# Optimization experiments

Measured on AMD Instinct MI355X. Metric: run time of the kernel, lower is better.

The kernel has to match this reference:

```python
import jax, jax.numpy as jnp
import numpy as np

ATOL = 1e-06
RTOL = 1e-06

def setup_inputs() -> dict:
    key = jax.random.key(0)
    ks = jax.random.split(key, 8)
    u = lambda k, shape: jax.random.uniform(k, shape, jnp.float32, -0.05, 0.05)
    return {
        "x": jax.random.normal(ks[0], (4096, 32, 32, 3), jnp.float32),
        "W_lstm": u(ks[1], (3, 16)),      # input kernel, gates [i,f,c,o]
        "U_lstm": u(ks[2], (4, 16)),      # recurrent kernel
        "dw_kernel": u(ks[3], (27, 27, 3, 5)),  # depthwise (kh,kw,in_c,mult)
        "pw_kernel": u(ks[4], (15, 4)),   # pointwise
        "conv_bias": u(ks[5], (4,)),
        "W_td": u(ks[6], (4096, 10)),
        "W_sc": u(ks[7], (4096, 10)),
    }

def _lstm_td(x, W, U):
    # TimeDistributed LSTM: x (B,32,32,3) -> treat axis1 as TD batch, axis2 as time
    B = x.shape[0]
    seq = x.reshape(B * 32, 32, 3)          # (N, T, F)
    xs = jnp.transpose(seq, (1, 0, 2))      # (T, N, F)
    N = seq.shape[0]
    h0 = jnp.zeros((N, 4), x.dtype)
    c0 = jnp.zeros((N, 4), x.dtype)

    def step(carry, xt):
        h, c = carry
        z = xt @ W + h @ U                  # (N, 16)
        zi, zf, zc, zo = jnp.split(z, 4, axis=-1)
        i = jax.nn.elu(zi)                  # recurrent_activation='elu'
        f = jax.nn.elu(zf)
        c = f * c + i * jax.nn.softmax(zc, axis=-1)  # activation='softmax'
        o = jax.nn.elu(zo)
        h = o * jax.nn.softmax(c, axis=-1)
        return (h, c), h

    _, hs = jax.lax.scan(step, (h0, c0), xs)        # (T, N, 4)
    return jnp.transpose(hs, (1, 0, 2)).reshape(B, 32, 32, 4)

def _sep_conv(x, dw_kernel, pw_kernel, conv_bias):
    # depthwise: Keras (kh,kw,C,M) -> lax HWIO grouped (kh,kw,1,C*M), channel-major order
    dw = dw_kernel.reshape(27, 27, 1, 15)
    y = jax.lax.conv_general_dilated(
        x, dw, window_strides=(1, 1), padding='SAME',
        feature_group_count=3,
        dimension_numbers=('NHWC', 'HWIO', 'NHWC'))   # (B,32,32,15)
    y = jnp.einsum('bhwc,cf->bhwf', y, pw_kernel) + conv_bias
    return jax.nn.sigmoid(y)                          # (B,32,32,4)

def reference(x, W_lstm, U_lstm, dw_kernel, pw_kernel, conv_bias, W_td, W_sc):
    B = x.shape[0]
    td = _lstm_td(x, W_lstm, U_lstm).reshape(B, -1) @ W_td   # (B,10)
    sc = _sep_conv(x, dw_kernel, pw_kernel, conv_bias).reshape(B, -1) @ W_sc
    diff = jnp.abs(td - sc)
    tol = ATOL + RTOL * jnp.abs(sc)
    return diff <= tol
```

## Files before the change

kernel.cpp:

```cpp
#include <hip/hip_runtime.h>
#include <math.h>

#define TD_OFF 0
#define WTDR_OFF 40960
#define SC_OFF 81920
#define BG_BYTE_OFF 524288

typedef __bf16 bf16x8 __attribute__((ext_vector_type(8)));
typedef float f32x16 __attribute__((ext_vector_type(16)));
typedef float f32x2 __attribute__((ext_vector_type(2)));

union FragU { bf16x8 v; float4 f; };

__device__ __forceinline__ f32x16 mfma16(bf16x8 a, bf16x8 b, f32x16 c) {
    return __builtin_amdgcn_mfma_f32_32x32x16_bf16(a, b, c, 0, 0, 0);
}

__device__ __forceinline__ float eluf(float v) {
    return v > 0.f ? v : __expf(v) - 1.f;
}

__global__ __launch_bounds__(256) void prep(const float* __restrict__ dw,
                                            const float* __restrict__ pw,
                                            const float* __restrict__ Wtd,
                                            float* __restrict__ Wtdr,
                                            unsigned short* __restrict__ Bg) {
    int gid = blockIdx.x * 256 + threadIdx.x;
    if (gid < 40960) {
        int k = gid & 3;
        int r = gid >> 2;
        int row = r & 31; r >>= 5;
        int j = r % 10;
        int tt = r / 10;
        Wtdr[gid] = Wtd[(size_t)(row * 128 + tt * 4 + k) * 10 + j];
        return;
    }
    int g2 = gid - 40960;
    if (g2 >= 162 * 128) return;
    int n = g2 & 127;
    int s = g2 >> 7;
    int half = s & 1;
    int cd = s >> 1;
    int c = cd / 27, d = cd % 27;
    int w = n >> 2, f = n & 3;
    unsigned short* dsth = Bg + (size_t)s * 4096 + n * 16;
    unsigned short* dstl = dsth + 2048;
#pragma unroll
    for (int k = 0; k < 16; k++) {
        int xi = half * 16 + k;
        int dx = xi - w + 13;
        float v = 0.f;
        if (dx >= 0 && dx < 27) {
#pragma unroll
            for (int m = 0; m < 5; m++)
                v = fmaf(dw[((d * 27 + dx) * 3 + c) * 5 + m],
                         pw[(c * 5 + m) * 4 + f], v);
        }
        __bf16 h = (__bf16)v;
        __bf16 l = (__bf16)(v - (float)h);
        dsth[k] = __builtin_bit_cast(unsigned short, h);
        dstl[k] = __builtin_bit_cast(unsigned short, l);
    }
}

#define A_OFF 0
#define ZOFF 49152
#define SRED_OFF 49168
#define LDS_BYTES 49808

__global__ __launch_bounds__(256, 3) void fused(const float* __restrict__ x,
                                                const float* __restrict__ W,
                                                const float* __restrict__ U,
                                                const float* __restrict__ Wtdr,
                                                const unsigned short* __restrict__ Bg,
                                                const float* __restrict__ Wsc,
                                                const float* __restrict__ bias,
                                                float* __restrict__ td_out,
                                                float* __restrict__ sc_out) {
    __shared__ char LDS[LDS_BYTES] __attribute__((aligned(16)));
    int bx = blockIdx.x;
    int rem = bx % 3;
    int q = bx / 3;
    int t = threadIdx.x;

    if (rem == 2) {
        f32x2 sW0[8], sW1[8], sW2[8], sU0[8], sU1[8], sU2[8], sU3[8];
        const f32x2* Wp = (const f32x2*)W;
        const f32x2* Up = (const f32x2*)U;
#pragma unroll
        for (int k2 = 0; k2 < 8; k2++) {
            sW0[k2] = Wp[k2];
            sW1[k2] = Wp[8 + k2];
            sW2[k2] = Wp[16 + k2];
            sU0[k2] = Up[k2];
            sU1[k2] = Up[8 + k2];
            sU2[k2] = Up[16 + k2];
            sU3[k2] = Up[24 + k2];
        }

        int n = q * 256 + t;
        int row = n & 31;
        const float4* xp4 = (const float4*)(x + (size_t)n * 96);

        float h0 = 0, h1 = 0, h2 = 0, h3 = 0;
        float c0 = 0, c1 = 0, c2 = 0, c3 = 0;
        f32x2 pa2[10];
#pragma unroll
        for (int j = 0; j < 10; j++) pa2[j] = 0.f;

        for (int g = 0; g < 8; g++) {
            float4 q0 = xp4[g * 3 + 0], q1 = xp4[g * 3 + 1], q2 = xp4[g * 3 + 2];
            float xr[12] = {q0.x, q0.y, q0.z, q0.w, q1.x, q1.y,
                            q1.z, q1.w, q2.x, q2.y, q2.z, q2.w};
#pragma unroll
            for (int st = 0; st < 4; st++) {
                int tt = g * 4 + st;
                float x0 = xr[st * 3 + 0], x1 = xr[st * 3 + 1], x2 = xr[st * 3 + 2];
                f32x2 z2[8];
#pragma unroll
                for (int k2 = 0; k2 < 8; k2++)
                    z2[k2] = sW0[k2] * x0 + sW1[k2] * x1 + sW2[k2] * x2
                           + sU0[k2] * h0 + sU1[k2] * h1 + sU2[k2] * h2
                           + sU3[k2] * h3;

                float ig0 = eluf(z2[0][0]), ig1 = eluf(z2[0][1]);
                float ig2 = eluf(z2[1][0]), ig3 = eluf(z2[1][1]);
                float fg0 = eluf(z2[2][0]), fg1 = eluf(z2[2][1]);
                float fg2 = eluf(z2[3][0]), fg3 = eluf(z2[3][1]);
                float og0 = eluf(z2[6][0]), og1 = eluf(z2[6][1]);
                float og2 = eluf(z2[7][0]), og3 = eluf(z2[7][1]);

                float zc0 = z2[4][0], zc1 = z2[4][1], zc2 = z2[5][0], zc3 = z2[5][1];
                float zm = fmaxf(fmaxf(zc0, zc1), fmaxf(zc2, zc3));
                float e0 = __expf(zc0 - zm), e1 = __expf(zc1 - zm);
                float e2 = __expf(zc2 - zm), e3 = __expf(zc3 - zm);
                float inv = 1.f / (e0 + e1 + e2 + e3);
                c0 = fg0 * c0 + ig0 * (e0 * inv);
                c1 = fg1 * c1 + ig1 * (e1 * inv);
                c2 = fg2 * c2 + ig2 * (e2 * inv);
                c3 = fg3 * c3 + ig3 * (e3 * inv);

                float cm = fmaxf(fmaxf(c0, c1), fmaxf(c2, c3));
                float p0 = __expf(c0 - cm), p1 = __expf(c1 - cm);
                float p2 = __expf(c2 - cm), p3 = __expf(c3 - cm);
                float pinv = 1.f / (p0 + p1 + p2 + p3);
                h0 = og0 * (p0 * pinv); h1 = og1 * (p1 * pinv);
                h2 = og2 * (p2 * pinv); h3 = og3 * (p3 * pinv);

                const f32x2* wr2 = (const f32x2*)(Wtdr + (size_t)tt * 1280) + row * 2;
                f32x2 h01 = {h0, h1}, h23 = {h2, h3};
#pragma unroll
                for (int j = 0; j < 10; j++)
                    pa2[j] += h01 * wr2[j * 64] + h23 * wr2[j * 64 + 1];
            }
        }

        float acc[10];
#pragma unroll
        for (int j = 0; j < 10; j++) acc[j] = pa2[j][0] + pa2[j][1];
#pragma unroll
        for (int off = 16; off >= 1; off >>= 1) {
#pragma unroll
            for (int j = 0; j < 10; j++) acc[j] += __shfl_xor(acc[j], off, 64);
        }
        int lane = t & 63;
        if (lane == 0 || lane == 32) {
            int b = n >> 5;
#pragma unroll
            for (int j = 0; j < 10; j++) td_out[b * 10 + j] = acc[j];
        }
        return;
    }

    int ci = q * 2 + rem;
    int l = t & 63;
    int wv = t >> 6;
    int m = l & 31;
    int sub = l >> 5;

    const char* bbase = (const char*)Bg + (size_t)wv * 1024 + m * 32 + sub * 16;
    FragU bA[4], bB[4];
#define LOADB2(OFF, arr) { const char* p_ = bbase + (OFF);                   \
        arr[0].f = *(const float4*)(p_);                          \
        arr[1].f = *(const float4*)(p_ + 4096);                   \
        arr[2].f = *(const float4*)(p_ + 8192);                   \
        arr[3].f = *(const float4*)(p_ + 12288); }

    LOADB2(0, bA);
    LOADB2(16384, bB);
    int boff = 2 * 16384;

    const float* xb = x + (size_t)ci * 12288;
#pragma unroll
    for (int rep = 0; rep < 2; rep++) {
        int u = rep * 256 + t;
        int im = u >> 7;
        int woct = (u >> 5) & 3;
        int h = u & 31;
        const float4* src = (const float4*)(xb + im * 3072 + h * 96 + woct * 24);
        float xr[24];
#pragma unroll
        for (int i = 0; i < 6; i++) {
            float4 qv = src[i];
            xr[i * 4 + 0] = qv.x; xr[i * 4 + 1] = qv.y;
            xr[i * 4 + 2] = qv.z; xr[i * 4 + 3] = qv.w;
        }
#pragma unroll
        for (int cc = 0; cc < 3; cc++) {
            FragU hiF, loF;
#pragma unroll
            for (int k = 0; k < 8; k++) {
                float v = xr[k * 3 + cc];
                __bf16 hb = (__bf16)v;
                hiF.v[k] = hb;
                loF.v[k] = (__bf16)(v - (float)hb);
            }
            int rec = A_OFF + im * 12288 + (cc * 8 + woct) * 512 + h * 16;
            *(float4*)(LDS + rec) = hiF.f;
            *(float4*)(LDS + rec + 2048) = loF.f;
        }
    }
    if (t < 4) *(float*)(LDS + ZOFF + t * 4) = 0.f;
    __syncthreads();

    f32x16 acc0 = {0,0,0,0,0,0,0,0,0,0,0,0,0,0,0,0};
    f32x16 acc1 = acc0, acc2 = acc0, acc3 = acc0;

    int c = 0, d = 0;

#define DCHUNK(BUF, DOLOAD) {                                                 \
    int rowIdx = m + d - 13;                                                  \
    bool valid = (unsigned)rowIdx < 32u;                                      \
    int a0 = A_OFF + (c * 8 + sub) * 512 + rowIdx * 16;                       \
    FragU f0h, f0l, f1h, f1l, g0h, g0l, g1h, g1l;                             \
    f0h.f = *(const float4*)(LDS + (valid ? a0          : ZOFF));             \
    f0l.f = *(const float4*)(LDS + (valid ? a0 + 2048   : ZOFF));             \
    f1h.f = *(const float4*)(LDS + (valid ? a0 + 1024   : ZOFF));             \
    f1l.f = *(const float4*)(LDS + (valid ? a0 + 3072   : ZOFF));             \
    g0h.f = *(const float4*)(LDS + (valid ? a0 + 12288  : ZOFF));             \
    g0l.f = *(const float4*)(LDS + (valid ? a0 + 14336  : ZOFF));             \
    g1h.f = *(const float4*)(LDS + (valid ? a0 + 13312  : ZOFF));             \
    g1l.f = *(const float4*)(LDS + (valid ? a0 + 15360  : ZOFF));             \
    acc0 = mfma16(f0h.v, BUF[0].v, acc0);                                     \
    acc1 = mfma16(g0h.v, BUF[0].v, acc1);                                     \
    acc0 = mfma16(f1h.v, BUF[2].v, acc0);                                     \
    acc1 = mfma16(g1h.v, BUF[2].v, acc1);                                     \
    acc0 = mfma16(f0h.v, BUF[1].v, acc0);                                     \
    acc1 = mfma16(g0h.v, BUF[1].v, acc1);                                     \
    acc0 = mfma16(f1h.v, BUF[3].v, acc0);                                     \
    acc1 = mfma16(g1h.v, BUF[3].v, acc1);                                     \
    acc0 = mfma16(f0l.v, BUF[0].v, acc0);                                     \
    acc1 = mfma16(g0l.v, BUF[0].v, acc1);                                     \
    acc0 = mfma16(f1l.v, BUF[2].v, acc0);                                     \
    acc1 = mfma16(g1l.v, BUF[2].v, acc1);                                     \
    if (DOLOAD) { LOADB2(boff, BUF); boff += 16384; }                         \
    f0h.f = *(const float4*)(LDS + (valid ? a0 + 24576  : ZOFF));             \
    f0l.f = *(const float4*)(LDS + (valid ? a0 + 26624  : ZOFF));             \
    f1h.f = *(const float4*)(LDS + (valid ? a0 + 25600  : ZOFF));             \
    f1l.f = *(const float4*)(LDS + (valid ? a0 + 27648  : ZOFF));             \
    g0h.f = *(const float4*)(LDS + (valid ? a0 + 36864  : ZOFF));             \
    g0l.f = *(const float4*)(LDS + (valid ? a0 + 38912  : ZOFF));             \
    g1h.f = *(const float4*)(LDS + (valid ? a0 + 37888  : ZOFF));             \
    g1l.f = *(const float4*)(LDS + (valid ? a0 + 39936  : ZOFF));             \
    acc2 = mfma16(f0h.v, BUF[0].v, acc2);                                     \
    acc3 = mfma16(g0h.v, BUF[0].v, acc3);                                     \
    acc2 = mfma16(f1h.v, BUF[2].v, acc2);                                     \
    acc3 = mfma16(g1h.v, BUF[2].v, acc3);                                     \
    acc2 = mfma16(f0h.v, BUF[1].v, acc2);                                     \
    acc3 = mfma16(g0h.v, BUF[1].v, acc3);                                     \
    acc2 = mfma16(f1h.v, BUF[3].v, acc2);                                     \
    acc3 = mfma16(g1h.v, BUF[3].v, acc3);                                     \
    acc2 = mfma16(f0l.v, BUF[0].v, acc2);                                     \
    acc3 = mfma16(g0l.v, BUF[0].v, acc3);                                     \
    acc2 = mfma16(f1l.v, BUF[2].v, acc2);                                     \
    acc3 = mfma16(g1l.v, BUF[2].v, acc3);                                     \
    d++; if (d == 27) { d = 0; c++; }                                         \
}

    for (int g = 0; g < 40; g++) {
        DCHUNK(bA, 1);
        DCHUNK(bB, 1);
    }
    DCHUNK(bA, 0);

    float b4[4];
#pragma unroll
    for (int i = 0; i < 4; i++) b4[i] = bias[i];

    float part[4][10];
#pragma unroll
    for (int i = 0; i < 4; i++)
#pragma unroll
        for (int j = 0; j < 10; j++) part[i][j] = 0.f;

    f32x16 accs[4] = {acc0, acc1, acc2, acc3};
    int ncol = wv * 32 + m;
    int wcol = ncol >> 2;
    int f = ncol & 3;
#pragma unroll
    for (int r = 0; r < 16; r++) {
        int h = (r & 3) + 8 * (r >> 2) + 4 * sub;
        const float* wr = Wsc + (size_t)((h * 32 + wcol) * 4 + f) * 10;
        float wreg[10];
#pragma unroll
        for (int j = 0; j < 10; j++) wreg[j] = wr[j];
#pragma unroll
        for (int im = 0; im < 4; im++) {
            float v = accs[im][r] + b4[f];
            float sg = 1.f / (1.f + __expf(-v));
#pragma unroll
            for (int j = 0; j < 10; j++) part[im][j] = fmaf(sg, wreg[j], part[im][j]);
        }
    }

#pragma unroll
    for (int off = 32; off >= 1; off >>= 1) {
#pragma unroll
        for (int im = 0; im < 4; im++)
#pragma unroll
            for (int j = 0; j < 10; j++) part[im][j] += __shfl_xor(part[im][j], off, 64);
    }
    if (l == 0) {
        float* red = (float*)(LDS + SRED_OFF);
#pragma unroll
        for (int im = 0; im < 4; im++)
#pragma unroll
            for (int j = 0; j < 10; j++) red[(wv * 4 + im) * 10 + j] = part[im][j];
    }
    __syncthreads();
    if (t < 40) {
        int img = t / 10, j = t % 10;
        const float* red = (const float*)(LDS + SRED_OFF);
        float sv = red[(0 * 4 + img) * 10 + j] + red[(1 * 4 + img) * 10 + j]
                 + red[(2 * 4 + img) * 10 + j] + red[(3 * 4 + img) * 10 + j];
        sc_out[(ci * 4 + img) * 10 + j] = sv;
    }
}

__global__ __launch_bounds__(256) void cmp_k(const float* __restrict__ td,
                                             const float* __restrict__ sc,
                                             float* __restrict__ out) {
    int i = blockIdx.x * 256 + threadIdx.x;
    if (i < 40960) {
        float a = td[i];
        float s = sc[i];
        float tol = 1e-6f + 1e-6f * fabsf(s);
        out[i] = (fabsf(a - s) <= tol) ? 1.0f : 0.0f;
    }
}

extern "C" void kernel_launch(void* const* d_in, const int* in_sizes, int n_in,
                              void* d_out, int out_size, void* d_ws, size_t ws_size,
                              hipStream_t stream) {
    const float* x    = (const float*)d_in[0];
    const float* W    = (const float*)d_in[1];
    const float* U    = (const float*)d_in[2];
    const float* dw   = (const float*)d_in[3];
    const float* pw   = (const float*)d_in[4];
    const float* bias = (const float*)d_in[5];
    const float* Wtd  = (const float*)d_in[6];
    const float* Wsc  = (const float*)d_in[7];

    float* ws     = (float*)d_ws;
    float* td_acc = ws + TD_OFF;
    float* Wtdr   = ws + WTDR_OFF;
    float* sc_acc = ws + SC_OFF;
    unsigned short* Bg = (unsigned short*)((char*)d_ws + BG_BYTE_OFF);

    prep<<<241, 256, 0, stream>>>(dw, pw, Wtd, Wtdr, Bg);
    fused<<<1536, 256, 0, stream>>>(x, W, U, Wtdr, Bg, Wsc, bias, td_acc, sc_acc);
    cmp_k<<<160, 256, 0, stream>>>(td_acc, sc_acc, (float*)d_out);
}
```

Baseline: 352.9 us.

## Split conv K-loop across two wave halves in 512-thread blocks with LDS reduction

Doubles the block size to 512 threads and splits the 81-step depthwise-conv K dimension between two groups of four waves: one handles chunks 0-40, the other chunks 41-80. The partial MFMA accumulators are reduced through LDS in two phases, and only the first group runs the sigmoid/Wsc epilogue. The LSTM blocks now process 512 sequences each, and the grid is rebalanced to a 4:1 conv-to-LSTM ratio. The aim is more parallelism and shorter per-wave serial chains. The cost is extra barriers, the LDS exchange, and higher register pressure under launch_bounds(512,4).

```diff
diff --git a/kernel.cpp b/kernel.cpp
--- a/kernel.cpp
+++ b/kernel.cpp
@@ -68,7 +68,7 @@
 #define SRED_OFF 49168
 #define LDS_BYTES 49808
 
-__global__ __launch_bounds__(256, 3) void fused(const float* __restrict__ x,
+__global__ __launch_bounds__(512, 4) void fused(const float* __restrict__ x,
                                                 const float* __restrict__ W,
                                                 const float* __restrict__ U,
                                                 const float* __restrict__ Wtdr,
@@ -79,11 +79,11 @@
                                                 float* __restrict__ sc_out) {
     __shared__ char LDS[LDS_BYTES] __attribute__((aligned(16)));
     int bx = blockIdx.x;
-    int rem = bx % 3;
-    int q = bx / 3;
+    int rem = bx % 5;
+    int q = bx / 5;
     int t = threadIdx.x;
 
-    if (rem == 2) {
+    if (rem == 4) {
         f32x2 sW0[8], sW1[8], sW2[8], sU0[8], sU1[8], sU2[8], sU3[8];
         const f32x2* Wp = (const f32x2*)W;
         const f32x2* Up = (const f32x2*)U;
@@ -98,7 +98,7 @@
             sU3[k2] = Up[24 + k2];
         }
 
-        int n = q * 256 + t;
+        int n = q * 512 + t;
         int row = n & 31;
         const float4* xp4 = (const float4*)(x + (size_t)n * 96);
 
@@ -172,13 +172,15 @@
         return;
     }
 
-    int ci = q * 2 + rem;
+    int ci = q * 4 + rem;
     int l = t & 63;
     int wv = t >> 6;
+    int kh = wv >> 2;
+    int nt = wv & 3;
     int m = l & 31;
     int sub = l >> 5;
 
-    const char* bbase = (const char*)Bg + (size_t)wv * 1024 + m * 32 + sub * 16;
+    const char* bbase = (const char*)Bg + (size_t)nt * 1024 + m * 32 + sub * 16;
     FragU bA[4], bB[4];
 #define LOADB2(OFF, arr) { const char* p_ = bbase + (OFF);                   \
         arr[0].f = *(const float4*)(p_);                          \
@@ -186,14 +188,14 @@
         arr[2].f = *(const float4*)(p_ + 8192);                   \
         arr[3].f = *(const float4*)(p_ + 12288); }
 
-    LOADB2(0, bA);
-    LOADB2(16384, bB);
-    int boff = 2 * 16384;
+    int cd0 = kh ? 41 : 0;
+    LOADB2((size_t)cd0 * 16384, bA);
+    LOADB2((size_t)(cd0 + 1) * 16384, bB);
+    size_t boff = (size_t)(cd0 + 2) * 16384;
 
     const float* xb = x + (size_t)ci * 12288;
-#pragma unroll
-    for (int rep = 0; rep < 2; rep++) {
-        int u = rep * 256 + t;
+    {
+        int u = t;
         int im = u >> 7;
         int woct = (u >> 5) & 3;
         int h = u & 31;
@@ -226,9 +228,10 @@
     f32x16 acc0 = {0,0,0,0,0,0,0,0,0,0,0,0,0,0,0,0};
     f32x16 acc1 = acc0, acc2 = acc0, acc3 = acc0;
 
-    int c = 0, d = 0;
-
-#define DCHUNK(BUF, DOLOAD) {                                                 \
+    int c = kh ? 1 : 0;
+    int d = kh ? 14 : 0;
+
+#define DCHUNK(BUF) {                                                         \
     int rowIdx = m + d - 13;                                                  \
     bool valid = (unsigned)rowIdx < 32u;                                      \
     int a0 = A_OFF + (c * 8 + sub) * 512 + rowIdx * 16;                       \
@@ -253,7 +256,7 @@
     acc1 = mfma16(g0l.v, BUF[0].v, acc1);                                     \
     acc0 = mfma16(f1l.v, BUF[2].v, acc0);                                     \
     acc1 = mfma16(g1l.v, BUF[2].v, acc1);                                     \
-    if (DOLOAD) { LOADB2(boff, BUF); boff += 16384; }                         \
+    LOADB2(boff, BUF); boff += 16384;                                         \
     f0h.f = *(const float4*)(LDS + (valid ? a0 + 24576  : ZOFF));             \
     f0l.f = *(const float4*)(LDS + (valid ? a0 + 26624  : ZOFF));             \
     f1h.f = *(const float4*)(LDS + (valid ? a0 + 25600  : ZOFF));             \
@@ -277,55 +280,107 @@
     d++; if (d == 27) { d = 0; c++; }                                         \
 }
 
-    for (int g = 0; g < 40; g++) {
-        DCHUNK(bA, 1);
-        DCHUNK(bB, 1);
-    }
-    DCHUNK(bA, 0);
-
-    float b4[4];
-#pragma unroll
-    for (int i = 0; i < 4; i++) b4[i] = bias[i];
-
-    float part[4][10];
-#pragma unroll
-    for (int i = 0; i < 4; i++)
-#pragma unroll
-        for (int j = 0; j < 10; j++) part[i][j] = 0.f;
+    for (int g = 0; g < 20; g++) {
+        DCHUNK(bA);
+        DCHUNK(bB);
+    }
+    if (kh == 0) DCHUNK(bA);
 
     f32x16 accs[4] = {acc0, acc1, acc2, acc3};
-    int ncol = wv * 32 + m;
-    int wcol = ncol >> 2;
-    int f = ncol & 3;
-#pragma unroll
-    for (int r = 0; r < 16; r++) {
-        int h = (r & 3) + 8 * (r >> 2) + 4 * sub;
-        const float* wr = Wsc + (size_t)((h * 32 + wcol) * 4 + f) * 10;
-        float wreg[10];
-#pragma unroll
-        for (int j = 0; j < 10; j++) wreg[j] = wr[j];
-#pragma unroll
-        for (int im = 0; im < 4; im++) {
-            float v = accs[im][r] + b4[f];
-            float sg = 1.f / (1.f + __expf(-v));
-#pragma unroll
-            for (int j = 0; j < 10; j++) part[im][j] = fmaf(sg, wreg[j], part[im][j]);
-        }
-    }
-
-#pragma unroll
-    for (int off = 32; off >= 1; off >>= 1) {
-#pragma unroll
-        for (int im = 0; im < 4; im++)
-#pragma unroll
-            for (int j = 0; j < 10; j++) part[im][j] += __shfl_xor(part[im][j], off, 64);
-    }
-    if (l == 0) {
-        float* red = (float*)(LDS + SRED_OFF);
-#pragma unroll
-        for (int im = 0; im < 4; im++)
-#pragma unroll
-            for (int j = 0; j < 10; j++) red[(wv * 4 + im) * 10 + j] = part[im][j];
+    float4* xch = (float4*)(LDS + A_OFF);
+    __syncthreads();
+    if (kh == 1 && nt < 2) {
+        float4* dst = xch + nt * 1024 + l;
+#pragma unroll
+        for (int i = 0; i < 4; i++)
+#pragma unroll
+            for (int rq = 0; rq < 4; rq++) {
+                float4 v = {accs[i][rq * 4 + 0], accs[i][rq * 4 + 1],
+                            accs[i][rq * 4 + 2], accs[i][rq * 4 + 3]};
+                dst[(i * 4 + rq) * 64] = v;
+            }
+    }
+    __syncthreads();
+    if (kh == 0 && nt < 2) {
+        const float4* src = xch + nt * 1024 + l;
+#pragma unroll
+        for (int i = 0; i < 4; i++)
+#pragma unroll
+            for (int rq = 0; rq < 4; rq++) {
+                float4 v = src[(i * 4 + rq) * 64];
+                accs[i][rq * 4 + 0] += v.x; accs[i][rq * 4 + 1] += v.y;
+                accs[i][rq * 4 + 2] += v.z; accs[i][rq * 4 + 3] += v.w;
+            }
+    }
+    __syncthreads();
+    if (kh == 1 && nt >= 2) {
+        float4* dst = xch + (nt - 2) * 1024 + l;
+#pragma unroll
+        for (int i = 0; i < 4; i++)
+#pragma unroll
+            for (int rq = 0; rq < 4; rq++) {
+                float4 v = {accs[i][rq * 4 + 0], accs[i][rq * 4 + 1],
+                            accs[i][rq * 4 + 2], accs[i][rq * 4 + 3]};
+                dst[(i * 4 + rq) * 64] = v;
+            }
+    }
+    __syncthreads();
+    if (kh == 0 && nt >= 2) {
+        const float4* src = xch + (nt - 2) * 1024 + l;
+#pragma unroll
+        for (int i = 0; i < 4; i++)
+#pragma unroll
+            for (int rq = 0; rq < 4; rq++) {
+                float4 v = src[(i * 4 + rq) * 64];
+                accs[i][rq * 4 + 0] += v.x; accs[i][rq * 4 + 1] += v.y;
+                accs[i][rq * 4 + 2] += v.z; accs[i][rq * 4 + 3] += v.w;
+            }
+    }
+
+    if (kh == 0) {
+        float b4[4];
+#pragma unroll
+        for (int i = 0; i < 4; i++) b4[i] = bias[i];
+
+        float part[4][10];
+#pragma unroll
+        for (int i = 0; i < 4; i++)
+#pragma unroll
+            for (int j = 0; j < 10; j++) part[i][j] = 0.f;
+
+        int ncol = nt * 32 + m;
+        int wcol = ncol >> 2;
+        int f = ncol & 3;
+#pragma unroll
+        for (int r = 0; r < 16; r++) {
+            int h = (r & 3) + 8 * (r >> 2) + 4 * sub;
+            const float* wr = Wsc + (size_t)((h * 32 + wcol) * 4 + f) * 10;
+            float wreg[10];
+#pragma unroll
+            for (int j = 0; j < 10; j++) wreg[j] = wr[j];
+#pragma unroll
+            for (int im = 0; im < 4; im++) {
+                float v = accs[im][r] + b4[f];
+                float sg = 1.f / (1.f + __expf(-v));
+#pragma unroll
+                for (int j = 0; j < 10; j++) part[im][j] = fmaf(sg, wreg[j], part[im][j]);
+            }
+        }
+
+#pragma unroll
+        for (int off = 32; off >= 1; off >>= 1) {
+#pragma unroll
+            for (int im = 0; im < 4; im++)
+#pragma unroll
+                for (int j = 0; j < 10; j++) part[im][j] += __shfl_xor(part[im][j], off, 64);
+        }
+        if (l == 0) {
+            float* red = (float*)(LDS + SRED_OFF);
+#pragma unroll
+            for (int im = 0; im < 4; im++)
+#pragma unroll
+                for (int j = 0; j < 10; j++) red[(nt * 4 + im) * 10 + j] = part[im][j];
+        }
     }
     __syncthreads();
     if (t < 40) {
@@ -368,6 +423,6 @@
     unsigned short* Bg = (unsigned short*)((char*)d_ws + BG_BYTE_OFF);
 
     prep<<<241, 256, 0, stream>>>(dw, pw, Wtd, Wtdr, Bg);
-    fused<<<1536, 256, 0, stream>>>(x, W, U, Wtdr, Bg, Wsc, bias, td_acc, sc_acc);
+    fused<<<1280, 512, 0, stream>>>(x, W, U, Wtdr, Bg, Wsc, bias, td_acc, sc_acc);
     cmp_k<<<160, 256, 0, stream>>>(td_acc, sc_acc, (float*)d_out);
 }
```

New measurement: 404.1 us. 14.5% more time.
